# Optimization experiments

Hardware: AMD Instinct MI355X
Metric: run time of the kernel (lower is better)

The kernel has to match this reference:

```python
import jax, jax.numpy as jnp
import numpy as np

SAMPLE_RATE = 16000
FRAME_LENGTH = 64
ATTENUATE_GAIN = 0.02
CHUNK_SIZE = 1000
TWO_PI = 2.0 * np.pi


def setup_inputs() -> dict:
    key = jax.random.key(0)
    k1, k2, k3 = jax.random.split(key, 3)
    b, v, h, f = 2, 8, 64, 500
    # fundamental frequencies in a musical range [80, 780) Hz
    frequencies = jax.random.uniform(k1, (b, v, f), dtype=jnp.float32) * 700.0 + 80.0
    harmonics = jax.random.uniform(k2, (b, v, h, f), dtype=jnp.float32)
    amplitude = jax.random.uniform(k3, (b, v, f), dtype=jnp.float32)
    return {"frequencies": frequencies, "harmonics": harmonics, "amplitude": amplitude}


def safe_divide(num, den, eps=1e-7):
    return num / jnp.where(den == 0.0, eps, den)


def linear_resample(x, n_t):
    # x: [N, F, H] -> [N, n_t, H]; bilinear, align_corners=False (half-pixel)
    F = x.shape[1]
    t = (jnp.arange(n_t, dtype=x.dtype) + 0.5) * (F / n_t) - 0.5
    t = jnp.clip(t, 0.0, F - 1.0)
    i0 = jnp.floor(t).astype(jnp.int32)
    i1 = jnp.minimum(i0 + 1, F - 1)
    w = (t - i0.astype(x.dtype))[None, :, None]
    return jnp.take(x, i0, axis=1) * (1.0 - w) + jnp.take(x, i1, axis=1) * w


def upsample_with_windows(x, n_t):
    # x: [N, F, C] -> [N, n_t, C]; overlapping Hann windows, add_endpoint=True
    x = jnp.concatenate([x, x[:, -1:]], axis=1)          # [N, F+1, C]
    n_frames = x.shape[1]
    hop = n_t // (n_frames - 1)
    wlen = 2 * hop
    win = 0.5 - 0.5 * jnp.cos(TWO_PI * jnp.arange(wlen, dtype=x.dtype) / wlen)  # periodic hann
    xw = x[:, :, :, None] * win                          # [N, F+1, C, 2*hop]
    N, Fp, C, _ = xw.shape
    a = xw[..., :hop].transpose(0, 2, 1, 3).reshape(N, C, Fp * hop)
    b = xw[..., hop:].transpose(0, 2, 1, 3).reshape(N, C, Fp * hop)
    out = jnp.zeros((N, C, (Fp + 1) * hop), dtype=x.dtype)
    out = out.at[:, :, : Fp * hop].add(a)
    out = out.at[:, :, hop:].add(b)
    out = out[:, :, hop:-hop]                            # trim rise/fall -> length n_t
    return out.transpose(0, 2, 1)


def angular_cumsum(omega, chunk=CHUNK_SIZE):
    # omega: [N, T, H]; chunked cumsum with mod-2pi stitching
    N, T, H = omega.shape
    pad = (chunk - T % chunk) % chunk
    if pad:
        omega = jnp.pad(omega, ((0, 0), (0, pad), (0, 0)))
    L = omega.shape[1]
    nc = L // chunk
    chunks = omega.reshape(N, nc, chunk, H)
    phase = jnp.cumsum(chunks, axis=2)
    offsets = phase[:, :, -1:, :] % TWO_PI
    offsets = jnp.concatenate([jnp.zeros_like(offsets[:, :1]), offsets[:, :-1]], axis=1)
    offsets = jnp.cumsum(offsets, axis=1) % TWO_PI
    phase = (phase + offsets) % TWO_PI
    return phase.reshape(N, L, H)[:, :T]


def reference(frequencies, harmonics, amplitude):
    b, v, frames = frequencies.shape
    n_h = harmonics.shape[2]
    n_samples = frames * FRAME_LENGTH
    nyquist = SAMPLE_RATE / 2.0

    harm = jnp.transpose(harmonics, (0, 1, 3, 2))              # [b, v, frames, n_h]
    ratios = jnp.linspace(1.0, float(n_h), n_h, dtype=frequencies.dtype)
    harm_freqs = frequencies[..., None] * ratios               # [b, v, frames, n_h]

    # normalize_below_nyquist: zero harmonics above nyquist, renormalize distribution
    harm = jnp.where(harm_freqs > nyquist, 0.0, harm)
    harm = safe_divide(harm, jnp.sum(harm, axis=-1, keepdims=True))
    harm_amps = amplitude[..., None] * harm                    # [b, v, frames, n_h]

    hf = harm_freqs.reshape(b * v, frames, n_h)
    ha = harm_amps.reshape(b * v, frames, n_h)
    freq_env = linear_resample(hf, n_samples)                  # [b*v, n_samples, n_h]
    amp_env = upsample_with_windows(ha, n_samples)             # [b*v, n_samples, n_h]

    # oscillator bank
    amp_env = jnp.where(freq_env > nyquist, 0.0, amp_env)
    omega = freq_env * (TWO_PI / SAMPLE_RATE)
    phase = angular_cumsum(omega)                              # use_angular_cumsum=True
    audio = jnp.sum(jnp.sin(phase) * amp_env, axis=-1)         # [b*v, n_samples]
    audio = audio.reshape(b, v, n_samples).sum(axis=1)         # sum voices -> [b, n_samples]
    return audio * ATTENUATE_GAIN
```

## Files before the change

kernel.cpp:

```cpp
#include <hip/hip_runtime.h>
#include <math.h>

#define NB 2
#define NVOICE 8
#define NN (NB * NVOICE)
#define NH 64
#define NF 500
#define NT 32000
#define NWIN 500
#define WIN 64

constexpr double kPIO2 = 1.5707963267948966;
constexpr double d_cos_red(double r) {
    double r2 = r * r, term = 1.0, sum = 1.0;
    for (int k = 1; k <= 12; ++k) { term *= -r2 / (double)((2 * k - 1) * (2 * k)); sum += term; }
    return sum;
}
constexpr double d_sin_red(double r) {
    double r2 = r * r, term = r, sum = r;
    for (int k = 1; k <= 12; ++k) { term *= -r2 / (double)((2 * k) * (2 * k + 1)); sum += term; }
    return sum;
}
constexpr double d_cos(double x) {
    int k = 0; double r = x;
    while (r > kPIO2 * 0.5) { r -= kPIO2; ++k; }
    switch (k & 3) {
        case 0: return d_cos_red(r);
        case 1: return -d_sin_red(r);
        case 2: return -d_cos_red(r);
        default: return d_sin_red(r);
    }
}
struct WinT { float wA[64]; float wB[64]; };
constexpr WinT make_win() {
    WinT w{};
    for (int j = 0; j < 64; ++j) {
        float aA = (float)6.283185307179586 * (float)j * 0.0078125f;
        float aB = (float)6.283185307179586 * (float)(j + 64) * 0.0078125f;
        w.wA[j] = 0.5f - 0.5f * (float)d_cos((double)aA);
        w.wB[j] = 0.5f - 0.5f * (float)d_cos((double)aB);
    }
    return w;
}
constexpr WinT WT = make_win();

template<int CTRL, int RMASK>
static __device__ __forceinline__ float dpp0_add(float x) {
    int y = __builtin_amdgcn_update_dpp(0, __float_as_int(x), CTRL, RMASK, 0xF, true);
    return x + __int_as_float(y);
}
static __device__ __forceinline__ float wave_incl_scan(float x) {
    x = dpp0_add<0x111, 0xF>(x);
    x = dpp0_add<0x112, 0xF>(x);
    x = dpp0_add<0x114, 0xF>(x);
    x = dpp0_add<0x118, 0xF>(x);
    x = dpp0_add<0x142, 0xa>(x);
    x = dpp0_add<0x143, 0xc>(x);
    return x;
}
static __device__ __forceinline__ float wave_sum_all_f(float x) {
    #pragma unroll
    for (int m = 1; m < 64; m <<= 1) x += __shfl_xor(x, m, 64);
    return x;
}
static __device__ __forceinline__ double wave_sum_all_d(double x) {
    #pragma unroll
    for (int m = 1; m < 64; m <<= 1) x += __shfl_xor(x, m, 64);
    return x;
}

__global__ __launch_bounds__(512) void ksyn_all(const float* __restrict__ freqs,
                                                const float* __restrict__ harms,
                                                const float* __restrict__ amps,
                                                float* __restrict__ out) {
    int q = blockIdx.x % NWIN;
    int b = blockIdx.x / NWIN;
    int tid = threadIdx.x;
    int v = tid >> 6, l = tid & 63;
    int n = (b << 3) + v;

    __shared__ float2 pb[NVOICE][NH];
    __shared__ float vsum[NVOICE][WIN];

    int f1 = (q + 1 < NF) ? q + 1 : NF - 1;
    const float* __restrict__ fr = freqs + n * NF;

    double D0;
    {
        double accd = 0.0;
        for (int j0 = 0; j0 < q; j0 += 64) {
            int j = j0 + l;
            float fv = (j < q) ? fr[j] : 0.0f;
            accd += (double)fv;
        }
        double S = wave_sum_all_d(accd);
        D0 = 64.0 * S;
        if (q > 0) D0 += 8.0 * ((double)fr[q] - (double)fr[q - 1]);
    }

    {
        int h = l;
        float kf = (float)(h + 1);
        const float* __restrict__ hb = harms + ((size_t)n * NH + h) * NF;
        float fq0 = fr[q], fq1 = fr[f1];
        float hm0 = hb[q], hm1 = hb[f1];
        hm0 = (__fmul_rn(fq0, kf) > 8000.0f) ? 0.0f : hm0;
        hm1 = (__fmul_rn(fq1, kf) > 8000.0f) ? 0.0f : hm1;
        float d0 = wave_sum_all_f(hm0), d1 = wave_sum_all_f(hm1);
        d0 = (d0 == 0.0f) ? 1e-7f : d0;
        d1 = (d1 == 0.0f) ? 1e-7f : d1;
        float va0 = amps[n * NF + q], va1 = amps[n * NF + f1];
        float a0 = __fmul_rn(va0, __fdiv_rn(hm0, d0));
        float a1 = __fmul_rn(va1, __fdiv_rn(hm1, d1));
        pb[v][h] = make_float2(a1, a0);
    }

    float vAu = fr[(q > 0) ? q - 1 : 0];
    float vBu = fr[q];
    float vCu = fr[f1];
    bool mlo   = (l < 32);
    bool mEdge = (q == 0 && mlo) || (q == NF - 1 && !mlo);
    float wy = (float)(mlo ? (2 * l + 65) : (2 * l - 63)) * 0.0078125f;
    float wx = 1.0f - wy;
    if (mEdge) { wx = 1.0f; wy = 0.0f; }
    float vLo0 = mEdge ? vBu : (mlo ? vAu : vBu);
    float vLo1 = mEdge ? vBu : (mlo ? vBu : vCu);
    float wA = WT.wA[l], wB = WT.wB[l];

    float feB = __fadd_rn(__fmul_rn(vLo0, wx), __fmul_rn(vLo1, wy));
    float scanB = wave_incl_scan(feB);

    float phiF;
    {
        double Phid = (D0 + (double)scanB) * (1.0 / 16000.0);
        Phid -= floor(Phid);
        phiF = (float)Phid;
    }
    float sp, cp;
    asm("v_sin_f32 %0, %1" : "=v"(sp) : "v"(phiF));
    asm("v_cos_f32 %0, %1" : "=v"(cp) : "v"(phiF));
    float c2 = __fadd_rn(cp, cp);

    float mxf = fmaxf(fmaxf(vAu, vBu), vCu);
    float mnf = fminf(fminf(vAu, vBu), vCu);
    int hmax = min(64, (int)(__fdiv_rn(8000.5f, mnf)));
    int hA   = min(hmax, (int)(__fdiv_rn(7999.96f, mxf)));
    hmax = __builtin_amdgcn_readfirstlane(hmax);
    hA   = __builtin_amdgcn_readfirstlane(hA);

    const float2* __restrict__ pbRow = pb[v];
    float accA = 0.0f, accB = 0.0f;
    float skm1 = 0.0f, sk = sp;
    int hh = 0;
    #pragma unroll 4
    for (; hh < hA; ++hh) {
        float2 a = pbRow[hh];
        accA = __fmaf_rn(sk, a.x, accA);
        accB = __fmaf_rn(sk, a.y, accB);
        float sn = __fmaf_rn(c2, sk, -skm1);
        skm1 = sk; sk = sn;
    }
    float kfv = (float)(hA + 1);
    #pragma unroll 4
    for (; hh < hmax; ++hh, kfv += 1.0f) {
        float2 a = pbRow[hh];
        float h0 = __fmul_rn(vLo0, kfv), h1 = __fmul_rn(vLo1, kfv);
        float fe = __fadd_rn(__fmul_rn(h0, wx), __fmul_rn(h1, wy));
        float sv = (fe > 8000.0f) ? 0.0f : sk;
        accA = __fmaf_rn(sv, a.x, accA);
        accB = __fmaf_rn(sv, a.y, accB);
        float sn = __fmaf_rn(c2, sk, -skm1);
        skm1 = sk; sk = sn;
    }
    vsum[v][l] = __fadd_rn(__fmul_rn(accA, wA), __fmul_rn(accB, wB));
    __syncthreads();

    if (tid < WIN) {
        float s8 = 0.0f;
        #pragma unroll
        for (int vv = 0; vv < NVOICE; ++vv) s8 = __fadd_rn(s8, vsum[vv][tid]);
        out[(size_t)b * NT + (q << 6) + tid] = __fmul_rn(0.02f, s8);
    }
}

extern "C" void kernel_launch(void* const* d_in, const int* in_sizes, int n_in,
                              void* d_out, int out_size, void* d_ws, size_t ws_size,
                              hipStream_t stream) {
    (void)in_sizes; (void)n_in; (void)out_size; (void)d_ws; (void)ws_size;
    const float* freqs = (const float*)d_in[0];
    const float* harms = (const float*)d_in[1];
    const float* amps  = (const float*)d_in[2];
    float* out = (float*)d_out;

    hipLaunchKernelGGL(ksyn_all, dim3(NB * NWIN), dim3(512), 0, stream,
                       freqs, harms, amps, out);
}
```

Before: 14.18 us.

## Process two output windows per block and reuse prefix sum and shared loads

Each block now handles a pair of adjacent 64-sample windows instead of one, so the grid halves to 500 blocks. The double-precision frequency prefix sum and the harmonic normalization for the shared middle frame are computed once per pair. The second window's phase offset comes from the last lane of the first window's scan. The harmonic-limit divisions also switch to hardware reciprocal-multiply, which is less exact and could shift the integer harmonic cutoffs at boundaries. The cost is fewer blocks to spread across CUs and more serial work per block.

```diff
diff --git a/kernel.cpp b/kernel.cpp
--- a/kernel.cpp
+++ b/kernel.cpp
@@ -7,7 +7,7 @@
 #define NH 64
 #define NF 500
 #define NT 32000
-#define NWIN 500
+#define NPAIR 250
 #define WIN 64
 
 constexpr double kPIO2 = 1.5707963267948966;
@@ -69,70 +69,26 @@
     return x;
 }
 
-__global__ __launch_bounds__(512) void ksyn_all(const float* __restrict__ freqs,
-                                                const float* __restrict__ harms,
-                                                const float* __restrict__ amps,
-                                                float* __restrict__ out) {
-    int q = blockIdx.x % NWIN;
-    int b = blockIdx.x / NWIN;
-    int tid = threadIdx.x;
-    int v = tid >> 6, l = tid & 63;
-    int n = (b << 3) + v;
-
-    __shared__ float2 pb[NVOICE][NH];
-    __shared__ float vsum[NVOICE][WIN];
-
-    int f1 = (q + 1 < NF) ? q + 1 : NF - 1;
-    const float* __restrict__ fr = freqs + n * NF;
-
-    double D0;
-    {
-        double accd = 0.0;
-        for (int j0 = 0; j0 < q; j0 += 64) {
-            int j = j0 + l;
-            float fv = (j < q) ? fr[j] : 0.0f;
-            accd += (double)fv;
-        }
-        double S = wave_sum_all_d(accd);
-        D0 = 64.0 * S;
-        if (q > 0) D0 += 8.0 * ((double)fr[q] - (double)fr[q - 1]);
-    }
-
-    {
-        int h = l;
-        float kf = (float)(h + 1);
-        const float* __restrict__ hb = harms + ((size_t)n * NH + h) * NF;
-        float fq0 = fr[q], fq1 = fr[f1];
-        float hm0 = hb[q], hm1 = hb[f1];
-        hm0 = (__fmul_rn(fq0, kf) > 8000.0f) ? 0.0f : hm0;
-        hm1 = (__fmul_rn(fq1, kf) > 8000.0f) ? 0.0f : hm1;
-        float d0 = wave_sum_all_f(hm0), d1 = wave_sum_all_f(hm1);
-        d0 = (d0 == 0.0f) ? 1e-7f : d0;
-        d1 = (d1 == 0.0f) ? 1e-7f : d1;
-        float va0 = amps[n * NF + q], va1 = amps[n * NF + f1];
-        float a0 = __fmul_rn(va0, __fdiv_rn(hm0, d0));
-        float a1 = __fmul_rn(va1, __fdiv_rn(hm1, d1));
-        pb[v][h] = make_float2(a1, a0);
-    }
-
-    float vAu = fr[(q > 0) ? q - 1 : 0];
-    float vBu = fr[q];
-    float vCu = fr[f1];
+static __device__ __forceinline__ float syn_window(int l,
+                                                   float vA, float vB, float vC,
+                                                   int edgeLo, int edgeHi,
+                                                   double Dstart, float wAv, float wBv,
+                                                   const float2* __restrict__ pbRow,
+                                                   float* __restrict__ vsDst) {
     bool mlo   = (l < 32);
-    bool mEdge = (q == 0 && mlo) || (q == NF - 1 && !mlo);
+    bool mEdge = (edgeLo && mlo) || (edgeHi && !mlo);
     float wy = (float)(mlo ? (2 * l + 65) : (2 * l - 63)) * 0.0078125f;
     float wx = 1.0f - wy;
     if (mEdge) { wx = 1.0f; wy = 0.0f; }
-    float vLo0 = mEdge ? vBu : (mlo ? vAu : vBu);
-    float vLo1 = mEdge ? vBu : (mlo ? vBu : vCu);
-    float wA = WT.wA[l], wB = WT.wB[l];
+    float vLo0 = mEdge ? vB : (mlo ? vA : vB);
+    float vLo1 = mEdge ? vB : (mlo ? vB : vC);
 
     float feB = __fadd_rn(__fmul_rn(vLo0, wx), __fmul_rn(vLo1, wy));
     float scanB = wave_incl_scan(feB);
 
     float phiF;
     {
-        double Phid = (D0 + (double)scanB) * (1.0 / 16000.0);
+        double Phid = (Dstart + (double)scanB) * (1.0 / 16000.0);
         Phid -= floor(Phid);
         phiF = (float)Phid;
     }
@@ -141,14 +97,16 @@
     asm("v_cos_f32 %0, %1" : "=v"(cp) : "v"(phiF));
     float c2 = __fadd_rn(cp, cp);
 
-    float mxf = fmaxf(fmaxf(vAu, vBu), vCu);
-    float mnf = fminf(fminf(vAu, vBu), vCu);
-    int hmax = min(64, (int)(__fdiv_rn(8000.5f, mnf)));
-    int hA   = min(hmax, (int)(__fdiv_rn(7999.96f, mxf)));
+    float mxf = fmaxf(fmaxf(vA, vB), vC);
+    float mnf = fminf(fminf(vA, vB), vC);
+    float rcm, rcx;
+    asm("v_rcp_f32 %0, %1" : "=v"(rcm) : "v"(mnf));
+    asm("v_rcp_f32 %0, %1" : "=v"(rcx) : "v"(mxf));
+    int hmax = min(64, (int)(__fmul_rn(8000.5f, rcm)));
+    int hA   = min(hmax, (int)(__fmul_rn(7999.9f, rcx)));
     hmax = __builtin_amdgcn_readfirstlane(hmax);
     hA   = __builtin_amdgcn_readfirstlane(hA);
 
-    const float2* __restrict__ pbRow = pb[v];
     float accA = 0.0f, accB = 0.0f;
     float skm1 = 0.0f, sk = sp;
     int hh = 0;
@@ -172,14 +130,80 @@
         float sn = __fmaf_rn(c2, sk, -skm1);
         skm1 = sk; sk = sn;
     }
-    vsum[v][l] = __fadd_rn(__fmul_rn(accA, wA), __fmul_rn(accB, wB));
+    *vsDst = __fadd_rn(__fmul_rn(accA, wAv), __fmul_rn(accB, wBv));
+    return scanB;
+}
+
+__global__ __launch_bounds__(512) void ksyn_all(const float* __restrict__ freqs,
+                                                const float* __restrict__ harms,
+                                                const float* __restrict__ amps,
+                                                float* __restrict__ out) {
+    int p = blockIdx.x % NPAIR;
+    int b = blockIdx.x / NPAIR;
+    int tid = threadIdx.x;
+    int v = tid >> 6, l = tid & 63;
+    int n = (b << 3) + v;
+
+    __shared__ float2 pb0[NVOICE][NH];
+    __shared__ float2 pb1[NVOICE][NH];
+    __shared__ float vsum[NVOICE][2 * WIN];
+
+    int q0 = p << 1, q1 = q0 + 1;
+    int f2 = (q1 + 1 < NF) ? q1 + 1 : NF - 1;
+    const float* __restrict__ fr = freqs + n * NF;
+
+    double D0;
+    {
+        double accd = 0.0;
+        for (int j0 = 0; j0 < q0; j0 += 64) {
+            int j = j0 + l;
+            float fv = (j < q0) ? fr[j] : 0.0f;
+            accd += (double)fv;
+        }
+        double S = wave_sum_all_d(accd);
+        D0 = 64.0 * S;
+        if (q0 > 0) D0 += 8.0 * ((double)fr[q0] - (double)fr[q0 - 1]);
+    }
+
+    float fq0 = fr[q0], fq1 = fr[q1], fq2 = fr[f2];
+    {
+        float kf = (float)(l + 1);
+        const float* __restrict__ hb = harms + ((size_t)n * NH + l) * NF;
+        float hm0 = hb[q0], hm1 = hb[q1], hm2 = hb[f2];
+        hm0 = (__fmul_rn(fq0, kf) > 8000.0f) ? 0.0f : hm0;
+        hm1 = (__fmul_rn(fq1, kf) > 8000.0f) ? 0.0f : hm1;
+        hm2 = (__fmul_rn(fq2, kf) > 8000.0f) ? 0.0f : hm2;
+        float d0 = wave_sum_all_f(hm0);
+        float d1 = wave_sum_all_f(hm1);
+        float d2 = wave_sum_all_f(hm2);
+        d0 = (d0 == 0.0f) ? 1e-7f : d0;
+        d1 = (d1 == 0.0f) ? 1e-7f : d1;
+        d2 = (d2 == 0.0f) ? 1e-7f : d2;
+        float va0 = amps[n * NF + q0], va1 = amps[n * NF + q1], va2 = amps[n * NF + f2];
+        float a0 = __fmul_rn(va0, __fdiv_rn(hm0, d0));
+        float a1 = __fmul_rn(va1, __fdiv_rn(hm1, d1));
+        float a2 = __fmul_rn(va2, __fdiv_rn(hm2, d2));
+        pb0[v][l] = make_float2(a1, a0);
+        pb1[v][l] = make_float2(a2, a1);
+    }
+
+    float wAv = WT.wA[l], wBv = WT.wB[l];
+    float vA0 = fr[(q0 > 0) ? q0 - 1 : 0];
+
+    float scan0 = syn_window(l, vA0, fq0, fq1, (q0 == 0), 0,
+                             D0, wAv, wBv, pb0[v], &vsum[v][l]);
+    double D1 = D0 + (double)__int_as_float(
+                    __builtin_amdgcn_readlane(__float_as_int(scan0), 63));
+    syn_window(l, fq0, fq1, fq2, 0, (q1 == NF - 1),
+               D1, wAv, wBv, pb1[v], &vsum[v][WIN + l]);
+
     __syncthreads();
 
-    if (tid < WIN) {
+    if (tid < 2 * WIN) {
         float s8 = 0.0f;
         #pragma unroll
         for (int vv = 0; vv < NVOICE; ++vv) s8 = __fadd_rn(s8, vsum[vv][tid]);
-        out[(size_t)b * NT + (q << 6) + tid] = __fmul_rn(0.02f, s8);
+        out[(size_t)b * NT + (p << 7) + tid] = __fmul_rn(0.02f, s8);
     }
 }
 
@@ -192,6 +216,6 @@
     const float* amps  = (const float*)d_in[2];
     float* out = (float*)d_out;
 
-    hipLaunchKernelGGL(ksyn_all, dim3(NB * NWIN), dim3(512), 0, stream,
+    hipLaunchKernelGGL(ksyn_all, dim3(NB * NPAIR), dim3(512), 0, stream,
                        freqs, harms, amps, out);
 }
```

Result: slower. 15.47 us (+9.0%).
